# Kernel tuning notes

Hardware: AMD Instinct MI355X
Metric: run time of the kernel (lower is better)

The kernel has to match this reference:

```python
import jax, jax.numpy as jnp
import numpy as np

D = 2048      # in_features (model dim)
H = 1408      # d_intermediate (hidden per expert)
E = 16        # n_routed_experts
T = 16384     # flattened tokens
K = 4         # top_k experts per token


def setup_inputs() -> dict:
    key = jax.random.key(0)
    k1, k2, k3, k4, k5 = jax.random.split(key, 5)
    x = jax.random.normal(k1, (T, D), dtype=jnp.float32)
    weights = jax.random.uniform(k2, (T, K), dtype=jnp.float32)
    indices = jax.random.randint(k3, (T, K), 0, E)
    # Stacked GatedMLP params (bias=False as in mamba's GatedMLP):
    # fc1: [2H, D] per expert, fc2: [D, H] per expert
    W1 = jax.random.normal(k4, (E, 2 * H, D), dtype=jnp.float32) * (D ** -0.5)
    W2 = jax.random.normal(k5, (E, D, H), dtype=jnp.float32) * (H ** -0.5)
    return {"x": x, "weights": weights, "indices": indices, "W1": W1, "W2": W2}


def reference(x, weights, indices, W1, W2):
    # y[t] = sum_i ( GatedMLP_i(x[t]) * sum_k weights[t,k] * [indices[t,k]==i] )
    n_experts = W1.shape[0]
    y = jnp.zeros_like(x)
    for i in range(n_experts):  # small fixed expert loop
        # combined routing weight of expert i per token (handles duplicate hits like += in torch)
        cw = jnp.sum(weights * (indices == i), axis=-1)      # [T]
        h = x @ W1[i].T                                      # [T, 2H]
        u, g = jnp.split(h, 2, axis=-1)                      # chunk(2, dim=-1): (y, gate)
        out = (u * jax.nn.silu(g)) @ W2[i].T                 # [T, D]
        y = y + out * cw[:, None]
    return y
```

## Files before the change

### kernel.cpp

```cpp
#include <hip/hip_runtime.h>

#define D_ 2048
#define H_ 1408
#define E_ 16
#define T_ 16384
#define K_ 4
#define TK_ 65536
#define BM_ 256
#define BK_ 64
#define MAXT_ 272
#define CVTB_ 408

typedef __attribute__((ext_vector_type(8))) short bf16x8;
typedef __attribute__((ext_vector_type(4))) float f32x4;
typedef __attribute__((ext_vector_type(4))) unsigned short u16x4;

#define M_NT     49
#define M_TE     64
#define M_TR     (64 + MAXT_)
#define M_TN     (64 + 2*MAXT_)

#define XB_OFF   0ULL
#define W1B_OFF  67108864ULL
#define W2B_OFF  (W1B_OFF + 188743680ULL)
#define ACT_OFF  (W2B_OFF + 94371840ULL)
#define PERM_OFF (ACT_OFF + 184549376ULL)
#define WGT_OFF  (PERM_OFF + 262144ULL)
#define META_B   (WGT_OFF + 262144ULL)

#define SBAR()  __builtin_amdgcn_s_barrier()
#define SCHED() __builtin_amdgcn_sched_barrier(0)
#define LGK0()  asm volatile("s_waitcnt lgkmcnt(0)" ::: "memory")
#define LGK2()  asm volatile("s_waitcnt lgkmcnt(2)" ::: "memory")
#define LGK4()  asm volatile("s_waitcnt lgkmcnt(4)" ::: "memory")
#define LGK6()  asm volatile("s_waitcnt lgkmcnt(6)" ::: "memory")
#define VM6()   asm volatile("s_waitcnt vmcnt(6)" ::: "memory")
#define PRIO1() __builtin_amdgcn_s_setprio(1)
#define PRIO0() __builtin_amdgcn_s_setprio(0)

static __device__ __forceinline__ unsigned short f2bf(float f) {
  unsigned u = __builtin_bit_cast(unsigned, f);
  u += 0x7fffu + ((u >> 16) & 1u);
  return (unsigned short)(u >> 16);
}

static __device__ __forceinline__ void gload16(const void* g, unsigned ldsOff) {
  __builtin_amdgcn_global_load_lds(
      (const __attribute__((address_space(1))) unsigned int*)(unsigned long long)g,
      (__attribute__((address_space(3))) unsigned int*)(unsigned long long)ldsOff,
      16, 0, 0);
}

__global__ __launch_bounds__(1024) void prep_kernel(
    const float* __restrict__ x, const float* __restrict__ W1,
    const int* __restrict__ idx, const float* __restrict__ wts,
    float* __restrict__ y, unsigned short* __restrict__ xb,
    unsigned short* __restrict__ w1b, int* __restrict__ meta,
    int* __restrict__ perm, float* __restrict__ wgt) {
  const int tid = threadIdx.x;
  if (blockIdx.x == gridDim.x - 1) {
    __shared__ int cnt[E_], cur[E_];
    if (tid < E_) cnt[tid] = 0;
    __syncthreads();
    for (int i = tid; i < TK_; i += 1024) atomicAdd(&cnt[idx[i]], 1);
    __syncthreads();
    if (tid == 0) {
      int off = 0, nt = 0;
      for (int e = 0; e < E_; ++e) {
        cur[e] = off;
        const int c = cnt[e];
        for (int r = 0; r < c; r += BM_) {
          meta[M_TE + nt] = e;
          meta[M_TR + nt] = off + r;
          meta[M_TN + nt] = (c - r < BM_) ? (c - r) : BM_;
          ++nt;
        }
        off += c;
      }
      meta[M_NT] = nt;
    }
    __syncthreads();
    for (int i = tid; i < TK_; i += 1024) {
      const int pos = atomicAdd(&cur[idx[i]], 1);
      perm[pos] = i >> 2;
      wgt[pos] = wts[i];
    }
    return;
  }
  const long long base = ((long long)blockIdx.x * 1024 + tid) * 4;
  const long long stride = (long long)(gridDim.x - 1) * 1024 * 4;
  for (long long i = base; i < (long long)T_ * D_; i += stride)
    *reinterpret_cast<float4*>(y + i) = (float4){0.f, 0.f, 0.f, 0.f};
  for (long long i = base; i < (long long)T_ * D_; i += stride) {
    float4 v = *reinterpret_cast<const float4*>(x + i);
    u16x4 o = { f2bf(v.x), f2bf(v.y), f2bf(v.z), f2bf(v.w) };
    *reinterpret_cast<u16x4*>(xb + i) = o;
  }
  for (long long i = base; i < (long long)E_ * 2 * H_ * D_; i += stride) {
    float4 v = *reinterpret_cast<const float4*>(W1 + i);
    u16x4 o = { f2bf(v.x), f2bf(v.y), f2bf(v.z), f2bf(v.w) };
    *reinterpret_cast<u16x4*>(w1b + i) = o;
  }
}

__global__ __launch_bounds__(512, 2) void gemm1_kernel(
    const char* __restrict__ xb, const char* __restrict__ w1b,
    const int* __restrict__ perm, const int* __restrict__ meta,
    unsigned short* __restrict__ act,
    const float* __restrict__ W2, unsigned short* __restrict__ w2b) {
  const int tid = threadIdx.x;
  const int bid0 = (int)blockIdx.x;
  if (bid0 < CVTB_) {
    long long i = ((long long)bid0 * 512 + tid) * 4;
    const long long stride = (long long)CVTB_ * 512 * 4;
    for (; i < (long long)E_ * D_ * H_; i += stride) {
      float4 v = *reinterpret_cast<const float4*>(W2 + i);
      u16x4 o = { f2bf(v.x), f2bf(v.y), f2bf(v.z), f2bf(v.w) };
      *reinterpret_cast<u16x4*>(w2b + i) = o;
    }
    return;
  }
  __shared__ char lds[131072];
  int bid = bid0 - CVTB_;
  bid = (bid & 7) * 374 + (bid >> 3);
  const int tb = bid / 11;
  const int cb = bid - tb * 11;
  if (tb >= meta[M_NT]) return;
  const int e = meta[M_TE + tb];
  const int row0 = meta[M_TR + tb];
  const int nrows = meta[M_TN + tb];
  const int lane = tid & 63, wid = tid >> 6;
  const int wr = wid >> 2, wc = wid & 3;
  const unsigned ldsBase = (unsigned)(unsigned long long)&lds[0];
  constexpr int NT = D_ / BK_;

  const char* aSrc[4];
  const char* bSrc[4];
  {
    const int r8 = tid >> 3;
    const unsigned colb0 = (unsigned)(tid & 7) * 16u;
#pragma unroll
    for (int i = 0; i < 4; ++i) {
      const int r = r8 + i * 64;
      const unsigned colb = colb0 ^ ((unsigned)(r & 7) << 4);
      const int rc = (r < nrows) ? r : 0;
      aSrc[i] = xb + (size_t)perm[row0 + rc] * 4096 + colb;
      const int w1row = (i < 2) ? (cb * 128 + r) : (H_ + cb * 128 + (r - 128));
      bSrc[i] = w1b + (size_t)e * (2 * H_) * 4096ULL + (size_t)w1row * 4096 + colb;
    }
  }

  const int l15 = lane & 15, hi = lane >> 4;
  const unsigned swz = (unsigned)(l15 & 7) << 4;
  unsigned aOff[8], bOffU[2], bOffG[2];
#pragma unroll
  for (int m = 0; m < 8; ++m) {
    const int row = wr * 128 + m * 16 + l15;
    aOff[m] = (unsigned)(row * 128) + (((unsigned)hi * 16u) ^ swz);
  }
#pragma unroll
  for (int n = 0; n < 2; ++n) {
    const int ru = wc * 32 + n * 16 + l15;
    bOffU[n] = 65536u + (unsigned)(ru * 128) + (((unsigned)hi * 16u) ^ swz);
    const int rg = ru + 128;
    bOffG[n] = 65536u + (unsigned)(rg * 128) + (((unsigned)hi * 16u) ^ swz);
  }

  f32x4 aU[8][2], aG[8][2];
#pragma unroll
  for (int m = 0; m < 8; ++m)
#pragma unroll
    for (int n = 0; n < 2; ++n) {
      aU[m][n] = (f32x4){0.f, 0.f, 0.f, 0.f};
      aG[m][n] = (f32x4){0.f, 0.f, 0.f, 0.f};
    }

  auto STAGE_A = [&](int t, int h) {
    const int tt = (t < NT) ? t : (NT - 1);
    const size_t kb = (size_t)tt * 128;
    const unsigned dst = ldsBase + (unsigned)(t & 1) * 32768u + (unsigned)h * 16384u + (unsigned)tid * 16u;
    gload16(aSrc[h * 2 + 0] + kb, dst);
    gload16(aSrc[h * 2 + 1] + kb, dst + 8192u);
  };
  auto STAGE_B = [&](int t, int h) {
    const int tt = (t < NT) ? t : (NT - 1);
    const size_t kb = (size_t)tt * 128;
    const unsigned dst = ldsBase + 65536u + (unsigned)(t & 1) * 32768u + (unsigned)h * 16384u + (unsigned)tid * 16u;
    gload16(bSrc[h * 2 + 0] + kb, dst);
    gload16(bSrc[h * 2 + 1] + kb, dst + 8192u);
  };

  STAGE_B(0, 0); STAGE_B(0, 1); STAGE_A(0, 0); STAGE_A(0, 1);
  STAGE_B(1, 0); STAGE_B(1, 1); STAGE_A(1, 0);
  VM6(); SCHED(); SBAR();

  bf16x8 aLo[4][2], aHi[4][2], bu[2][2], bg[2][2];
#pragma unroll
  for (int ks = 0; ks < 2; ++ks) {
#pragma unroll
    for (int m = 0; m < 4; ++m)
      aLo[m][ks] = *reinterpret_cast<const bf16x8*>(lds + (aOff[m] ^ (unsigned)(ks << 6)));
#pragma unroll
    for (int n = 0; n < 2; ++n)
      bu[n][ks] = *reinterpret_cast<const bf16x8*>(lds + (bOffU[n] ^ (unsigned)(ks << 6)));
  }

  for (int t = 0; t < NT; ++t) {
    const char* base = lds + (unsigned)(t & 1) * 32768u;
    const char* nbase = lds + (unsigned)((t + 1) & 1) * 32768u;

#pragma unroll
    for (int ks = 0; ks < 2; ++ks)
#pragma unroll
      for (int n = 0; n < 2; ++n)
        bg[n][ks] = *reinterpret_cast<const bf16x8*>(base + (bOffG[n] ^ (unsigned)(ks << 6)));
    STAGE_A(t + 1, 1);
    SCHED();
    PRIO1();
#pragma unroll
    for (int ks = 0; ks < 2; ++ks)
#pragma unroll
      for (int m = 0; m < 4; ++m)
#pragma unroll
        for (int n = 0; n < 2; ++n)
          aU[m][n] = __builtin_amdgcn_mfma_f32_16x16x32_bf16(aLo[m][ks], bu[n][ks], aU[m][n], 0, 0, 0);
    PRIO0(); SCHED(); SBAR();

#pragma unroll
    for (int ks = 0; ks < 2; ++ks)
#pragma unroll
      for (int m = 0; m < 4; ++m)
        aHi[m][ks] = *reinterpret_cast<const bf16x8*>(base + (aOff[4 + m] ^ (unsigned)(ks << 6)));
    STAGE_B(t + 2, 0);
    SCHED();
    PRIO1();
#pragma unroll
    for (int ks = 0; ks < 2; ++ks)
#pragma unroll
      for (int m = 0; m < 4; ++m)
#pragma unroll
        for (int n = 0; n < 2; ++n)
          aG[m][n] = __builtin_amdgcn_mfma_f32_16x16x32_bf16(aLo[m][ks], bg[n][ks], aG[m][n], 0, 0, 0);
    PRIO0(); SCHED(); SBAR();

    STAGE_B(t + 2, 1);
    SCHED();
    PRIO1();
#pragma unroll
    for (int ks = 0; ks < 2; ++ks)
#pragma unroll
      for (int m = 0; m < 4; ++m)
#pragma unroll
        for (int n = 0; n < 2; ++n)
          aU[4 + m][n] = __builtin_amdgcn_mfma_f32_16x16x32_bf16(aHi[m][ks], bu[n][ks], aU[4 + m][n], 0, 0, 0);
    PRIO0(); SCHED(); SBAR();

    STAGE_A(t + 2, 0);
    VM6(); SCHED(); SBAR();
#pragma unroll
    for (int ks = 0; ks < 2; ++ks) {
#pragma unroll
      for (int m = 0; m < 4; ++m)
        aLo[m][ks] = *reinterpret_cast<const bf16x8*>(nbase + (aOff[m] ^ (unsigned)(ks << 6)));
#pragma unroll
      for (int n = 0; n < 2; ++n)
        bu[n][ks] = *reinterpret_cast<const bf16x8*>(nbase + (bOffU[n] ^ (unsigned)(ks << 6)));
    }
    SCHED();
    PRIO1();
#pragma unroll
    for (int ks = 0; ks < 2; ++ks)
#pragma unroll
      for (int m = 0; m < 4; ++m)
#pragma unroll
        for (int n = 0; n < 2; ++n)
          aG[4 + m][n] = __builtin_amdgcn_mfma_f32_16x16x32_bf16(aHi[m][ks], bg[n][ks], aG[4 + m][n], 0, 0, 0);
    PRIO0(); SCHED();
  }

#pragma unroll
  for (int m = 0; m < 8; ++m)
#pragma unroll
    for (int j = 0; j < 4; ++j) {
      const int r = wr * 128 + m * 16 + hi * 4 + j;
      if (r < nrows) {
        const size_t rowBase = (size_t)(row0 + r) * H_ + (size_t)cb * 128 + (size_t)wc * 32;
#pragma unroll
        for (int n = 0; n < 2; ++n) {
          const float u = aU[m][n][j];
          const float g = aG[m][n][j];
          act[rowBase + n * 16 + l15] = f2bf(u * (g / (1.0f + __expf(-g))));
        }
      }
    }
}

__global__ __launch_bounds__(512, 2) void gemm2_kernel(
    const char* __restrict__ actb, const char* __restrict__ w2b,
    const int* __restrict__ perm, const float* __restrict__ wgt,
    const int* __restrict__ meta, float* __restrict__ y) {
  __shared__ char lds[131072];
  int bid = (int)blockIdx.x;
  bid = (bid & 7) * (int)(gridDim.x >> 3) + (bid >> 3);
  const int tb = bid >> 3;
  const int cb = bid & 7;
  if (tb >= meta[M_NT]) return;
  const int e = meta[M_TE + tb];
  const int row0 = meta[M_TR + tb];
  const int nrows = meta[M_TN + tb];
  const int tid = threadIdx.x, lane = tid & 63, wid = tid >> 6;
  const int wr = wid >> 2, wc = wid & 3;
  const unsigned ldsBase = (unsigned)(unsigned long long)&lds[0];
  constexpr int NT = H_ / BK_;

  const char* aSrc[4];
  const char* bSrc[4];
  {
    const int r8 = tid >> 3;
    const unsigned colb0 = (unsigned)(tid & 7) * 16u;
#pragma unroll
    for (int i = 0; i < 4; ++i) {
      const int r = r8 + i * 64;
      const unsigned colb = colb0 ^ ((unsigned)(r & 7) << 4);
      const int rc = (r < nrows) ? r : 0;
      aSrc[i] = actb + (size_t)(row0 + rc) * (H_ * 2) + colb;
      const int brow = cb * 256 + r;
      bSrc[i] = w2b + (size_t)e * D_ * (H_ * 2) + (size_t)brow * (H_ * 2) + colb;
    }
  }

  const int l15 = lane & 15, hi = lane >> 4;
  const unsigned swz = (unsigned)(l15 & 7) << 4;
  unsigned aOff[8], bOff[4];
#pragma unroll
  for (int m = 0; m < 8; ++m) {
    const int row = wr * 128 + m * 16 + l15;
    aOff[m] = (unsigned)(row * 128) + (((unsigned)hi * 16u) ^ swz);
  }
#pragma unroll
  for (int n = 0; n < 4; ++n) {
    const int rb = wc * 64 + n * 16 + l15;
    bOff[n] = 65536u + (unsigned)(rb * 128) + (((unsigned)hi * 16u) ^ swz);
  }

  f32x4 acc[8][4];
#pragma unroll
  for (int m = 0; m < 8; ++m)
#pragma unroll
    for (int n = 0; n < 4; ++n) acc[m][n] = (f32x4){0.f, 0.f, 0.f, 0.f};

  auto STAGE_A = [&](int t, int h) {
    const int tt = (t < NT) ? t : (NT - 1);
    const size_t kb = (size_t)tt * 128;
    const unsigned dst = ldsBase + (unsigned)(t & 1) * 32768u + (unsigned)h * 16384u + (unsigned)tid * 16u;
    gload16(aSrc[h * 2 + 0] + kb, dst);
    gload16(aSrc[h * 2 + 1] + kb, dst + 8192u);
  };
  auto STAGE_B = [&](int t, int h) {
    const int tt = (t < NT) ? t : (NT - 1);
    const size_t kb = (size_t)tt * 128;
    const unsigned dst = ldsBase + 65536u + (unsigned)(t & 1) * 32768u + (unsigned)h * 16384u + (unsigned)tid * 16u;
    gload16(bSrc[h * 2 + 0] + kb, dst);
    gload16(bSrc[h * 2 + 1] + kb, dst + 8192u);
  };

  STAGE_B(0, 0); STAGE_B(0, 1); STAGE_A(0, 0); STAGE_A(0, 1);
  STAGE_B(1, 0); STAGE_B(1, 1); STAGE_A(1, 0);
  VM6(); SCHED(); SBAR();

  for (int t = 0; t < NT; ++t) {
    const char* base = lds + (unsigned)(t & 1) * 32768u;
    bf16x8 aLo[4][2], aHi[4][2], b[4][2];

#pragma unroll
    for (int ks = 0; ks < 2; ++ks) {
#pragma unroll
      for (int m = 0; m < 4; ++m)
        aLo[m][ks] = *reinterpret_cast<const bf16x8*>(base + (aOff[m] ^ (unsigned)(ks << 6)));
#pragma unroll
      for (int n = 0; n < 2; ++n)
        b[n][ks] = *reinterpret_cast<const bf16x8*>(base + (bOff[n] ^ (unsigned)(ks << 6)));
    }
    STAGE_A(t + 1, 1);
    SCHED(); SBAR(); LGK6(); SCHED();
    PRIO1();
#pragma unroll
    for (int m = 0; m < 4; ++m)
#pragma unroll
      for (int n = 0; n < 2; ++n)
        acc[m][n] = __builtin_amdgcn_mfma_f32_16x16x32_bf16(aLo[m][0], b[n][0], acc[m][n], 0, 0, 0);
    LGK0(); SCHED();
#pragma unroll
    for (int m = 0; m < 4; ++m)
#pragma unroll
      for (int n = 0; n < 2; ++n)
        acc[m][n] = __builtin_amdgcn_mfma_f32_16x16x32_bf16(aLo[m][1], b[n][1], acc[m][n], 0, 0, 0);
    PRIO0(); SCHED(); SBAR();

#pragma unroll
    for (int ks = 0; ks < 2; ++ks)
#pragma unroll
      for (int n = 2; n < 4; ++n)
        b[n][ks] = *reinterpret_cast<const bf16x8*>(base + (bOff[n] ^ (unsigned)(ks << 6)));
    STAGE_B(t + 2, 0);
    SCHED(); SBAR(); LGK2(); SCHED();
    PRIO1();
#pragma unroll
    for (int m = 0; m < 4; ++m)
#pragma unroll
      for (int n = 2; n < 4; ++n)
        acc[m][n] = __builtin_amdgcn_mfma_f32_16x16x32_bf16(aLo[m][0], b[n][0], acc[m][n], 0, 0, 0);
    LGK0(); SCHED();
#pragma unroll
    for (int m = 0; m < 4; ++m)
#pragma unroll
      for (int n = 2; n < 4; ++n)
        acc[m][n] = __builtin_amdgcn_mfma_f32_16x16x32_bf16(aLo[m][1], b[n][1], acc[m][n], 0, 0, 0);
    PRIO0(); SCHED(); SBAR();

#pragma unroll
    for (int ks = 0; ks < 2; ++ks)
#pragma unroll
      for (int m = 0; m < 4; ++m)
        aHi[m][ks] = *reinterpret_cast<const bf16x8*>(base + (aOff[4 + m] ^ (unsigned)(ks << 6)));
    STAGE_B(t + 2, 1);
    SCHED(); SBAR(); LGK4(); SCHED();
    PRIO1();
#pragma unroll
    for (int m = 0; m < 4; ++m)
#pragma unroll
      for (int n = 0; n < 2; ++n)
        acc[4 + m][n] = __builtin_amdgcn_mfma_f32_16x16x32_bf16(aHi[m][0], b[n][0], acc[4 + m][n], 0, 0, 0);
    LGK0(); SCHED();
#pragma unroll
    for (int m = 0; m < 4; ++m)
#pragma unroll
      for (int n = 0; n < 2; ++n)
        acc[4 + m][n] = __builtin_amdgcn_mfma_f32_16x16x32_bf16(aHi[m][1], b[n][1], acc[4 + m][n], 0, 0, 0);
    PRIO0(); SCHED(); SBAR();

    STAGE_A(t + 2, 0);
    VM6(); SCHED(); SBAR();
    PRIO1();
#pragma unroll
    for (int ks = 0; ks < 2; ++ks)
#pragma unroll
      for (int m = 0; m < 4; ++m)
#pragma unroll
        for (int n = 2; n < 4; ++n)
          acc[4 + m][n] = __builtin_amdgcn_mfma_f32_16x16x32_bf16(aHi[m][ks], b[n][ks], acc[4 + m][n], 0, 0, 0);
    PRIO0(); SCHED(); SBAR();
  }

#pragma unroll
  for (int m = 0; m < 8; ++m)
#pragma unroll
    for (int j = 0; j < 4; ++j) {
      const int r = wr * 128 + m * 16 + hi * 4 + j;
      if (r < nrows) {
        const float w = wgt[row0 + r];
        const int token = perm[row0 + r];
        float* yrow = y + (size_t)token * D_ + (size_t)cb * 256 + (size_t)wc * 64;
#pragma unroll
        for (int n = 0; n < 4; ++n)
          unsafeAtomicAdd(&yrow[n * 16 + l15], acc[m][n][j] * w);
      }
    }
}

extern "C" void kernel_launch(void* const* d_in, const int* in_sizes, int n_in,
                              void* d_out, int out_size, void* d_ws, size_t ws_size,
                              hipStream_t stream) {
  const float* x   = (const float*)d_in[0];
  const float* wts = (const float*)d_in[1];
  const int*   idx = (const int*)d_in[2];
  const float* W1  = (const float*)d_in[3];
  const float* W2  = (const float*)d_in[4];
  float* y = (float*)d_out;
  char* ws = (char*)d_ws;

  unsigned short* xb  = (unsigned short*)(ws + XB_OFF);
  unsigned short* w1b = (unsigned short*)(ws + W1B_OFF);
  unsigned short* w2b = (unsigned short*)(ws + W2B_OFF);
  unsigned short* act = (unsigned short*)(ws + ACT_OFF);
  int*   perm = (int*)(ws + PERM_OFF);
  float* wgt  = (float*)(ws + WGT_OFF);
  int*   meta = (int*)(ws + META_B);

  prep_kernel<<<2049, 1024, 0, stream>>>(x, W1, idx, wts, y, xb, w1b, meta, perm, wgt);

  gemm1_kernel<<<CVTB_ + MAXT_ * (H_ / 128), 512, 0, stream>>>(
      (const char*)xb, (const char*)w1b, perm, meta, act, W2, w2b);

  gemm2_kernel<<<MAXT_ * (D_ / 256), 512, 0, stream>>>(
      (const char*)act, (const char*)w2b, perm, wgt, meta, y);
}
```

Before: 1.610 ms.

## Shrink gemm2 tiles to 128x128 with simple single-buffered loop

Replaces gemm2's 256x256 tile with a hand-scheduled double-buffered pipeline by 128x128 tiles on 256 threads, each 256-row token group split into two halves and one 32KB single-buffered LDS stage. Each K step waits for all loads, then computes, and the launch grid grows fourfold. The aim is more blocks for load balance and occupancy, and skipping half-tiles that hold no rows. In exchange, global loads no longer overlap compute within a block, and every K step rereads more W2 and activation data with less reuse.

Measured after the change: 1.571 ms. 2.4% less time.

```diff
diff --git a/kernel.cpp b/kernel.cpp
--- a/kernel.cpp
+++ b/kernel.cpp
@@ -30,10 +30,7 @@
 
 #define SBAR()  __builtin_amdgcn_s_barrier()
 #define SCHED() __builtin_amdgcn_sched_barrier(0)
-#define LGK0()  asm volatile("s_waitcnt lgkmcnt(0)" ::: "memory")
-#define LGK2()  asm volatile("s_waitcnt lgkmcnt(2)" ::: "memory")
-#define LGK4()  asm volatile("s_waitcnt lgkmcnt(4)" ::: "memory")
-#define LGK6()  asm volatile("s_waitcnt lgkmcnt(6)" ::: "memory")
+#define VM0()   asm volatile("s_waitcnt vmcnt(0)" ::: "memory")
 #define VM6()   asm volatile("s_waitcnt vmcnt(6)" ::: "memory")
 #define PRIO1() __builtin_amdgcn_s_setprio(1)
 #define PRIO0() __builtin_amdgcn_s_setprio(0)
@@ -295,21 +292,24 @@
     }
 }
 
-__global__ __launch_bounds__(512, 2) void gemm2_kernel(
+__global__ __launch_bounds__(256) void gemm2_kernel(
     const char* __restrict__ actb, const char* __restrict__ w2b,
     const int* __restrict__ perm, const float* __restrict__ wgt,
     const int* __restrict__ meta, float* __restrict__ y) {
-  __shared__ char lds[131072];
+  __shared__ char lds[32768];
   int bid = (int)blockIdx.x;
-  bid = (bid & 7) * (int)(gridDim.x >> 3) + (bid >> 3);
-  const int tb = bid >> 3;
-  const int cb = bid & 7;
+  bid = (bid & 7) * ((int)gridDim.x >> 3) + (bid >> 3);
+  const int st = bid >> 4;
+  const int cb = bid & 15;
+  const int tb = st >> 1, half = st & 1;
   if (tb >= meta[M_NT]) return;
+  const int nrA = meta[M_TN + tb] - half * 128;
+  if (nrA <= 0) return;
+  const int nrows = (nrA < 128) ? nrA : 128;
+  const int row0 = meta[M_TR + tb] + half * 128;
   const int e = meta[M_TE + tb];
-  const int row0 = meta[M_TR + tb];
-  const int nrows = meta[M_TN + tb];
   const int tid = threadIdx.x, lane = tid & 63, wid = tid >> 6;
-  const int wr = wid >> 2, wc = wid & 3;
+  const int wr = wid >> 1, wc = wid & 1;
   const unsigned ldsBase = (unsigned)(unsigned long long)&lds[0];
   constexpr int NT = H_ / BK_;
 
@@ -320,147 +320,74 @@
     const unsigned colb0 = (unsigned)(tid & 7) * 16u;
 #pragma unroll
     for (int i = 0; i < 4; ++i) {
-      const int r = r8 + i * 64;
+      const int r = r8 + i * 32;
       const unsigned colb = colb0 ^ ((unsigned)(r & 7) << 4);
       const int rc = (r < nrows) ? r : 0;
       aSrc[i] = actb + (size_t)(row0 + rc) * (H_ * 2) + colb;
-      const int brow = cb * 256 + r;
+      const int brow = cb * 128 + r;
       bSrc[i] = w2b + (size_t)e * D_ * (H_ * 2) + (size_t)brow * (H_ * 2) + colb;
     }
   }
 
   const int l15 = lane & 15, hi = lane >> 4;
   const unsigned swz = (unsigned)(l15 & 7) << 4;
-  unsigned aOff[8], bOff[4];
-#pragma unroll
-  for (int m = 0; m < 8; ++m) {
-    const int row = wr * 128 + m * 16 + l15;
-    aOff[m] = (unsigned)(row * 128) + (((unsigned)hi * 16u) ^ swz);
-  }
-#pragma unroll
-  for (int n = 0; n < 4; ++n) {
-    const int rb = wc * 64 + n * 16 + l15;
-    bOff[n] = 65536u + (unsigned)(rb * 128) + (((unsigned)hi * 16u) ^ swz);
-  }
-
-  f32x4 acc[8][4];
-#pragma unroll
-  for (int m = 0; m < 8; ++m)
+  unsigned aOff[4], bOff[4];
+#pragma unroll
+  for (int m = 0; m < 4; ++m) {
+    const int ra = wr * 64 + m * 16 + l15;
+    aOff[m] = (unsigned)(ra * 128) + (((unsigned)hi * 16u) ^ swz);
+    const int rb = wc * 64 + m * 16 + l15;
+    bOff[m] = 16384u + (unsigned)(rb * 128) + (((unsigned)hi * 16u) ^ swz);
+  }
+
+  f32x4 acc[4][4];
+#pragma unroll
+  for (int m = 0; m < 4; ++m)
 #pragma unroll
     for (int n = 0; n < 4; ++n) acc[m][n] = (f32x4){0.f, 0.f, 0.f, 0.f};
 
-  auto STAGE_A = [&](int t, int h) {
-    const int tt = (t < NT) ? t : (NT - 1);
-    const size_t kb = (size_t)tt * 128;
-    const unsigned dst = ldsBase + (unsigned)(t & 1) * 32768u + (unsigned)h * 16384u + (unsigned)tid * 16u;
-    gload16(aSrc[h * 2 + 0] + kb, dst);
-    gload16(aSrc[h * 2 + 1] + kb, dst + 8192u);
+  auto STAGE = [&](int t) {
+    const size_t kb = (size_t)t * 128;
+    const unsigned dst = ldsBase + (unsigned)tid * 16u;
+#pragma unroll
+    for (int i = 0; i < 4; ++i) {
+      gload16(aSrc[i] + kb, dst + (unsigned)i * 4096u);
+      gload16(bSrc[i] + kb, dst + 16384u + (unsigned)i * 4096u);
+    }
   };
-  auto STAGE_B = [&](int t, int h) {
-    const int tt = (t < NT) ? t : (NT - 1);
-    const size_t kb = (size_t)tt * 128;
-    const unsigned dst = ldsBase + 65536u + (unsigned)(t & 1) * 32768u + (unsigned)h * 16384u + (unsigned)tid * 16u;
-    gload16(bSrc[h * 2 + 0] + kb, dst);
-    gload16(bSrc[h * 2 + 1] + kb, dst + 8192u);
-  };
-
-  STAGE_B(0, 0); STAGE_B(0, 1); STAGE_A(0, 0); STAGE_A(0, 1);
-  STAGE_B(1, 0); STAGE_B(1, 1); STAGE_A(1, 0);
-  VM6(); SCHED(); SBAR();
-
+
+  STAGE(0);
   for (int t = 0; t < NT; ++t) {
-    const char* base = lds + (unsigned)(t & 1) * 32768u;
-    bf16x8 aLo[4][2], aHi[4][2], b[4][2];
-
+    VM0(); SCHED(); SBAR();
 #pragma unroll
     for (int ks = 0; ks < 2; ++ks) {
-#pragma unroll
-      for (int m = 0; m < 4; ++m)
-        aLo[m][ks] = *reinterpret_cast<const bf16x8*>(base + (aOff[m] ^ (unsigned)(ks << 6)));
-#pragma unroll
-      for (int n = 0; n < 2; ++n)
-        b[n][ks] = *reinterpret_cast<const bf16x8*>(base + (bOff[n] ^ (unsigned)(ks << 6)));
-    }
-    STAGE_A(t + 1, 1);
-    SCHED(); SBAR(); LGK6(); SCHED();
-    PRIO1();
-#pragma unroll
-    for (int m = 0; m < 4; ++m)
-#pragma unroll
-      for (int n = 0; n < 2; ++n)
-        acc[m][n] = __builtin_amdgcn_mfma_f32_16x16x32_bf16(aLo[m][0], b[n][0], acc[m][n], 0, 0, 0);
-    LGK0(); SCHED();
-#pragma unroll
-    for (int m = 0; m < 4; ++m)
-#pragma unroll
-      for (int n = 0; n < 2; ++n)
-        acc[m][n] = __builtin_amdgcn_mfma_f32_16x16x32_bf16(aLo[m][1], b[n][1], acc[m][n], 0, 0, 0);
-    PRIO0(); SCHED(); SBAR();
-
-#pragma unroll
-    for (int ks = 0; ks < 2; ++ks)
-#pragma unroll
-      for (int n = 2; n < 4; ++n)
-        b[n][ks] = *reinterpret_cast<const bf16x8*>(base + (bOff[n] ^ (unsigned)(ks << 6)));
-    STAGE_B(t + 2, 0);
-    SCHED(); SBAR(); LGK2(); SCHED();
-    PRIO1();
-#pragma unroll
-    for (int m = 0; m < 4; ++m)
-#pragma unroll
-      for (int n = 2; n < 4; ++n)
-        acc[m][n] = __builtin_amdgcn_mfma_f32_16x16x32_bf16(aLo[m][0], b[n][0], acc[m][n], 0, 0, 0);
-    LGK0(); SCHED();
-#pragma unroll
-    for (int m = 0; m < 4; ++m)
-#pragma unroll
-      for (int n = 2; n < 4; ++n)
-        acc[m][n] = __builtin_amdgcn_mfma_f32_16x16x32_bf16(aLo[m][1], b[n][1], acc[m][n], 0, 0, 0);
-    PRIO0(); SCHED(); SBAR();
-
-#pragma unroll
-    for (int ks = 0; ks < 2; ++ks)
-#pragma unroll
-      for (int m = 0; m < 4; ++m)
-        aHi[m][ks] = *reinterpret_cast<const bf16x8*>(base + (aOff[4 + m] ^ (unsigned)(ks << 6)));
-    STAGE_B(t + 2, 1);
-    SCHED(); SBAR(); LGK4(); SCHED();
-    PRIO1();
-#pragma unroll
-    for (int m = 0; m < 4; ++m)
-#pragma unroll
-      for (int n = 0; n < 2; ++n)
-        acc[4 + m][n] = __builtin_amdgcn_mfma_f32_16x16x32_bf16(aHi[m][0], b[n][0], acc[4 + m][n], 0, 0, 0);
-    LGK0(); SCHED();
-#pragma unroll
-    for (int m = 0; m < 4; ++m)
-#pragma unroll
-      for (int n = 0; n < 2; ++n)
-        acc[4 + m][n] = __builtin_amdgcn_mfma_f32_16x16x32_bf16(aHi[m][1], b[n][1], acc[4 + m][n], 0, 0, 0);
-    PRIO0(); SCHED(); SBAR();
-
-    STAGE_A(t + 2, 0);
-    VM6(); SCHED(); SBAR();
-    PRIO1();
-#pragma unroll
-    for (int ks = 0; ks < 2; ++ks)
-#pragma unroll
-      for (int m = 0; m < 4; ++m)
-#pragma unroll
-        for (int n = 2; n < 4; ++n)
-          acc[4 + m][n] = __builtin_amdgcn_mfma_f32_16x16x32_bf16(aHi[m][ks], b[n][ks], acc[4 + m][n], 0, 0, 0);
-    PRIO0(); SCHED(); SBAR();
-  }
-
-#pragma unroll
-  for (int m = 0; m < 8; ++m)
+      bf16x8 a[4], b[4];
+#pragma unroll
+      for (int m = 0; m < 4; ++m) {
+        a[m] = *reinterpret_cast<const bf16x8*>(lds + (aOff[m] ^ (unsigned)(ks << 6)));
+        b[m] = *reinterpret_cast<const bf16x8*>(lds + (bOff[m] ^ (unsigned)(ks << 6)));
+      }
+      PRIO1();
+#pragma unroll
+      for (int m = 0; m < 4; ++m)
+#pragma unroll
+        for (int n = 0; n < 4; ++n)
+          acc[m][n] = __builtin_amdgcn_mfma_f32_16x16x32_bf16(a[m], b[n], acc[m][n], 0, 0, 0);
+      PRIO0();
+    }
+    SCHED(); SBAR();
+    if (t + 1 < NT) STAGE(t + 1);
+  }
+
+#pragma unroll
+  for (int m = 0; m < 4; ++m)
 #pragma unroll
     for (int j = 0; j < 4; ++j) {
-      const int r = wr * 128 + m * 16 + hi * 4 + j;
+      const int r = wr * 64 + m * 16 + hi * 4 + j;
       if (r < nrows) {
         const float w = wgt[row0 + r];
         const int token = perm[row0 + r];
-        float* yrow = y + (size_t)token * D_ + (size_t)cb * 256 + (size_t)wc * 64;
+        float* yrow = y + (size_t)token * D_ + (size_t)cb * 128 + (size_t)wc * 64;
 #pragma unroll
         for (int n = 0; n < 4; ++n)
           unsafeAtomicAdd(&yrow[n * 16 + l15], acc[m][n][j] * w);
@@ -492,6 +419,6 @@
   gemm1_kernel<<<CVTB_ + MAXT_ * (H_ / 128), 512, 0, stream>>>(
       (const char*)xb, (const char*)w1b, perm, meta, act, W2, w2b);
 
-  gemm2_kernel<<<MAXT_ * (D_ / 256), 512, 0, stream>>>(
+  gemm2_kernel<<<MAXT_ * 2 * (D_ / 128), 256, 0, stream>>>(
       (const char*)act, (const char*)w2b, perm, wgt, meta, y);
 }
```
